# Performance work log

Measured on AMD Instinct MI355X. Metric: run time of the kernel, lower is better.

## Reference

```python
import jax, jax.numpy as jnp
import numpy as np

B = 131072
D_IN = 128
D_H = 128
DT = 1.0
LN_EPS = 1e-5


def setup_inputs() -> dict:
    key = jax.random.key(0)
    ks = jax.random.split(key, 12)
    s_in = 1.0 / np.sqrt(D_IN)
    s_h = 1.0 / np.sqrt(D_H)
    s_g = 1.0 / np.sqrt(D_IN + D_H)
    return {
        "x_t": jax.random.normal(ks[0], (B, D_IN), dtype=jnp.float32),
        "state": jax.random.normal(ks[1], (B, D_H), dtype=jnp.float32),
        "w_in": jax.random.uniform(ks[2], (D_H, D_IN), jnp.float32, -s_in, s_in),
        "b_in": jax.random.uniform(ks[3], (D_H,), jnp.float32, -s_in, s_in),
        "w_rec": jax.random.uniform(ks[4], (D_H, D_H), jnp.float32, -s_h, s_h),
        "w_gate": jax.random.uniform(ks[5], (D_H, D_IN + D_H), jnp.float32, -s_g, s_g),
        "b_gate": jax.random.uniform(ks[6], (D_H,), jnp.float32, -s_g, s_g),
        "bias": jnp.zeros((D_H,), jnp.float32),
        "log_step": jnp.zeros((D_H,), jnp.float32),
        "ln_gamma": jnp.ones((D_IN + D_H,), jnp.float32),
        "ln_beta": jnp.zeros((D_IN + D_H,), jnp.float32),
    }


def reference(x_t, state, w_in, b_in, w_rec, w_gate, b_gate, bias, log_step, ln_gamma, ln_beta):
    # per-unit learned time scale in (0, 1)
    step_size = jax.nn.sigmoid(log_step)  # [D_H]
    # drive = input_proj(x) + recurrent_proj(tanh(state)) + bias
    drive = (jnp.einsum("bi,hi->bh", x_t, w_in) + b_in
             + jnp.einsum("bj,hj->bh", jnp.tanh(state), w_rec)
             + bias)  # [B, D_H]
    # LayerNorm over concat([x, state])
    gi = jnp.concatenate([x_t, state], axis=-1)  # [B, D_IN+D_H]
    mu = jnp.mean(gi, axis=-1, keepdims=True)
    var = jnp.mean(jnp.square(gi - mu), axis=-1, keepdims=True)
    gi = (gi - mu) * jax.lax.rsqrt(var + LN_EPS) * ln_gamma + ln_beta
    gate = jax.nn.sigmoid(jnp.einsum("bk,hk->bh", gi, w_gate) + b_gate)  # [B, D_H]
    target = jnp.tanh(drive)
    blend = jnp.minimum(DT * step_size * gate, 1.0)
    new_state = state + blend * (target - state)
    return new_state
```

## Files before the change

### kernel.cpp

```cpp
#include <hip/hip_runtime.h>

#define D        128
#define M_TILE   32
#define THREADS  512
#define B_ROWS   131072
#define NTILES   (B_ROWS / M_TILE)
#define GRID     512

typedef __bf16  bf16x8  __attribute__((ext_vector_type(8)));
typedef float   f32x4   __attribute__((ext_vector_type(4)));

#define LOG2E 1.4426950408889634f
#define WS_FRAGS      4096
#define WS_PARAMS_OFF (2 * WS_FRAGS)
#define WS_NEEDED     (2 * WS_FRAGS * 16 + 128 * 16)

__device__ __forceinline__ float fexp2(float x) { return __builtin_amdgcn_exp2f(x); }
__device__ __forceinline__ float frcp(float x)  { return __builtin_amdgcn_rcpf(x); }

__device__ __forceinline__ float fast_tanh(float x) {
    float e = fexp2(x * (2.f * LOG2E));
    return 1.f - 2.f * frcp(e + 1.f);
}
__device__ __forceinline__ float fast_sigmoid(float x) {
    return frcp(1.f + fexp2(-LOG2E * x));
}

__global__ __launch_bounds__(THREADS)
void prep(const float* __restrict__ w_in,   const float* __restrict__ b_in,
          const float* __restrict__ w_rec,  const float* __restrict__ w_gate,
          const float* __restrict__ b_gate, const float* __restrict__ bias,
          const float* __restrict__ log_step,
          const float* __restrict__ gamma,  const float* __restrict__ beta,
          bf16x8* __restrict__ ws)
{
    const int bid = blockIdx.x, tid = threadIdx.x;
    if (bid < 8) {
        const int t    = bid * THREADS + tid;
        const int l    = t & 63;
        const int kb   = (t >> 6) & 7;
        const int w    = (t >> 9) & 7;
        const int hcol = w * 16 + (l & 15);
        const int k    = kb * 32 + ((l >> 4) & 3) * 8;
        bf16x8 fd, fg;
        const float* s1 = (k < 128) ? (w_in + hcol * 128 + k) : (w_rec + hcol * 128 + (k - 128));
        const float* s2 = w_gate + hcol * 256 + k;
        #pragma unroll
        for (int j = 0; j < 8; ++j) {
            fd[j] = (__bf16)s1[j];
            fg[j] = (__bf16)(s2[j] * gamma[k + j]);
        }
        ws[t]            = fd;
        ws[WS_FRAGS + t] = fg;
    } else {
        const int h   = tid >> 2;
        const int sub = tid & 3;
        float bacc = 0.f, csum = 0.f;
        const float* wp = w_gate + h * 256 + sub * 64;
        const float* gp = gamma + sub * 64;
        const float* bp = beta  + sub * 64;
        #pragma unroll
        for (int k = 0; k < 64; ++k) {
            const float wv = wp[k];
            bacc += wv * bp[k];
            csum += (float)(__bf16)(wv * gp[k]);
        }
        bacc += __shfl_xor(bacc, 1);
        bacc += __shfl_xor(bacc, 2);
        csum += __shfl_xor(csum, 1);
        csum += __shfl_xor(csum, 2);
        if (sub == 0) {
            f32x4 p;
            p[0] = fast_sigmoid(log_step[h]);
            p[1] = b_in[h] + bias[h];
            p[2] = b_gate[h] + bacc;
            p[3] = csum;
            *((f32x4*)(ws + WS_PARAMS_OFF) + h) = p;
        }
    }
}

__global__ __launch_bounds__(THREADS, 4)
void liquid_cell_ws(const float* __restrict__ x, const float* __restrict__ st,
                    const bf16x8* __restrict__ ws, float* __restrict__ out)
{
    __shared__ __align__(16) __bf16 XT[M_TILE * 128];
    __shared__ __align__(16) __bf16 TT[M_TILE * 128];
    __shared__ __align__(16) __bf16 SS[M_TILE * 128];
    __shared__ float2 MUB[M_TILE];

    const int tid  = threadIdx.x;
    const int lane = tid & 63;
    const int wave = tid >> 6;
    const int q    = lane >> 4;
    const int arow = lane & 15;
    const int hcol = wave * 16 + arow;
    const int koff = q * 8;
    const int fbase = wave * 512 + lane;

    const f32x4 pp = *((const f32x4*)(ws + WS_PARAMS_OFF) + hcol);
    const float stepv = pp[0], bd = pp[1], bg = pp[2], colsum = pp[3];

    const bf16x8* WD = ws;
    const bf16x8* WG = ws + WS_FRAGS;

    const int r    = tid >> 4;
    const int c0   = (tid & 15) * 8;
    const int sw   = (r & 7) << 3;
    const int rsw  = (arow & 7) << 3;

    for (int tile = blockIdx.x; tile < NTILES; tile += GRID) {
        const float* xp = x  + ((long)tile * M_TILE + r) * D + c0;
        const float* sp = st + ((long)tile * M_TILE + r) * D + c0;
        const f32x4 xa = *(const f32x4*)xp, xb = *(const f32x4*)(xp + 4);
        const f32x4 sa = *(const f32x4*)sp, sb = *(const f32x4*)(sp + 4);

        float sum = 0.f, sq = 0.f;
        #pragma unroll
        for (int j = 0; j < 4; ++j) {
            sum += xa[j] + xb[j] + sa[j] + sb[j];
            sq  += xa[j]*xa[j] + xb[j]*xb[j] + sa[j]*sa[j] + sb[j]*sb[j];
        }
        #pragma unroll
        for (int m = 1; m < 16; m <<= 1) {
            sum += __shfl_xor(sum, m);
            sq  += __shfl_xor(sq,  m);
        }
        const float mu   = sum * (1.f / 256.f);
        const float rstd = __builtin_amdgcn_rsqf(sq * (1.f / 256.f) - mu * mu + 1e-5f);

        bf16x8 fx, ft, fs;
        #pragma unroll
        for (int j = 0; j < 4; ++j) {
            fx[j]     = (__bf16)xa[j];
            fx[j + 4] = (__bf16)xb[j];
            ft[j]     = (__bf16)fast_tanh(sa[j]);
            ft[j + 4] = (__bf16)fast_tanh(sb[j]);
            fs[j]     = (__bf16)sa[j];
            fs[j + 4] = (__bf16)sb[j];
        }

        __syncthreads();
        *(bf16x8*)&XT[(r * 128 + c0) ^ sw] = fx;
        *(bf16x8*)&TT[(r * 128 + c0) ^ sw] = ft;
        *(bf16x8*)&SS[(r * 128 + c0) ^ sw] = fs;
        if ((tid & 15) == 0) MUB[r] = make_float2(mu * rstd, rstd);
        __syncthreads();

        bf16x8 fw[8], fv[8];
        #pragma unroll
        for (int kb = 0; kb < 8; ++kb) {
            fw[kb] = WG[fbase + kb * 64];
            fv[kb] = WD[fbase + kb * 64];
        }

        f32x4 acc2[2], acc1[2];
        acc2[0] = (f32x4)(0.f); acc2[1] = (f32x4)(0.f);
        acc1[0] = (f32x4)(0.f); acc1[1] = (f32x4)(0.f);
        #pragma unroll
        for (int ms = 0; ms < 2; ++ms) {
            const int base = (ms * 16 + arow) * 128;
            #pragma unroll
            for (int kb = 0; kb < 4; ++kb) {
                bf16x8 a = *(const bf16x8*)&XT[base + ((kb * 32 + koff) ^ rsw)];
                acc2[ms] = __builtin_amdgcn_mfma_f32_16x16x32_bf16(a, fw[kb], acc2[ms], 0, 0, 0);
                acc1[ms] = __builtin_amdgcn_mfma_f32_16x16x32_bf16(a, fv[kb], acc1[ms], 0, 0, 0);
            }
            #pragma unroll
            for (int kb = 0; kb < 4; ++kb) {
                bf16x8 s_ = *(const bf16x8*)&SS[base + ((kb * 32 + koff) ^ rsw)];
                acc2[ms] = __builtin_amdgcn_mfma_f32_16x16x32_bf16(s_, fw[kb + 4], acc2[ms], 0, 0, 0);
                bf16x8 t_ = *(const bf16x8*)&TT[base + ((kb * 32 + koff) ^ rsw)];
                acc1[ms] = __builtin_amdgcn_mfma_f32_16x16x32_bf16(t_, fv[kb + 4], acc1[ms], 0, 0, 0);
            }
        }

        const long obase = (long)tile * M_TILE;
        #pragma unroll
        for (int ms = 0; ms < 2; ++ms) {
            #pragma unroll
            for (int rg = 0; rg < 4; ++rg) {
                const int row = ms * 16 + q * 4 + rg;
                const float2 mr = MUB[row];
                const float gate   = fast_sigmoid(mr.y * acc2[ms][rg] - mr.x * colsum + bg);
                const float s      = (float)SS[(row * 128 + hcol) ^ ((row & 7) << 3)];
                const float target = fast_tanh(acc1[ms][rg] + bd);
                const float blend  = fminf(stepv * gate, 1.f);
                out[(obase + row) * D + hcol] = s + blend * (target - s);
            }
        }
    }
}

__global__ __launch_bounds__(THREADS, 4)
void liquid_cell_fb(const float* __restrict__ x,      const float* __restrict__ st,
                    const float* __restrict__ w_in,   const float* __restrict__ b_in,
                    const float* __restrict__ w_rec,  const float* __restrict__ w_gate,
                    const float* __restrict__ b_gate, const float* __restrict__ bias,
                    const float* __restrict__ log_step,
                    const float* __restrict__ gamma,  const float* __restrict__ beta,
                    float* __restrict__ out)
{
    __shared__ __align__(16) __bf16 A1[32 * 256];
    __shared__ __align__(16) __bf16 A2[32 * 256];
    __shared__ __align__(16) float  SBUF[32 * 128];

    const int tid  = threadIdx.x;
    const int lane = tid & 63;
    const int wave = tid >> 6;
    const int q    = lane >> 4;
    const int arow = lane & 15;
    const int hcol = wave * 16 + arow;
    const int koff = q * 8;

    const float stepv = fast_sigmoid(log_step[hcol]);
    const float bd    = b_in[hcol] + bias[hcol];
    float       bg    = b_gate[hcol];

    bf16x8 wd[8], wg[8];
    float betaAcc = 0.f;
    #pragma unroll
    for (int kb = 0; kb < 8; ++kb) {
        const int k = kb * 32 + koff;
        const float* s1 = (k < 128) ? (w_in  + hcol * 128 + k)
                                    : (w_rec + hcol * 128 + (k - 128));
        const float* s2 = w_gate + hcol * 256 + k;
        #pragma unroll
        for (int j = 0; j < 8; ++j) {
            wd[kb][j] = (__bf16)s1[j];
            const float wv = s2[j];
            wg[kb][j] = (__bf16)(wv * gamma[k + j]);
            betaAcc  += wv * beta[k + j];
        }
    }
    betaAcc += __shfl_xor(betaAcc, 16);
    betaAcc += __shfl_xor(betaAcc, 32);
    bg += betaAcc;

    const int r    = tid >> 4;
    const int c0   = (tid & 15) * 8;
    const int sw   = (r & 7) << 3;
    const int swf  = (r & 7) << 2;
    const int rsw  = (arow & 7) << 3;

    for (int tile = blockIdx.x; tile < (B_ROWS / 32); tile += GRID) {
        const float* xp = x  + ((long)tile * 32 + r) * D + c0;
        const float* sp = st + ((long)tile * 32 + r) * D + c0;
        const f32x4 xa = *(const f32x4*)xp, xb = *(const f32x4*)(xp + 4);
        const f32x4 sa = *(const f32x4*)sp, sb = *(const f32x4*)(sp + 4);

        float sum = 0.f, sq = 0.f;
        #pragma unroll
        for (int j = 0; j < 4; ++j) {
            sum += xa[j] + xb[j] + sa[j] + sb[j];
            sq  += xa[j]*xa[j] + xb[j]*xb[j] + sa[j]*sa[j] + sb[j]*sb[j];
        }
        #pragma unroll
        for (int m = 1; m < 16; m <<= 1) {
            sum += __shfl_xor(sum, m);
            sq  += __shfl_xor(sq,  m);
        }
        const float mu   = sum * (1.f / 256.f);
        const float rstd = __builtin_amdgcn_rsqf(sq * (1.f / 256.f) - mu * mu + 1e-5f);
        const float nmur = -mu * rstd;

        bf16x8 a1x, a1s, a2x, a2s;
        #pragma unroll
        for (int j = 0; j < 4; ++j) {
            a1x[j]     = (__bf16)xa[j];
            a1x[j + 4] = (__bf16)xb[j];
            a1s[j]     = (__bf16)fast_tanh(sa[j]);
            a1s[j + 4] = (__bf16)fast_tanh(sb[j]);
            a2x[j]     = (__bf16)(xa[j] * rstd + nmur);
            a2x[j + 4] = (__bf16)(xb[j] * rstd + nmur);
            a2s[j]     = (__bf16)(sa[j] * rstd + nmur);
            a2s[j + 4] = (__bf16)(sb[j] * rstd + nmur);
        }

        __syncthreads();
        *(bf16x8*)&A1[(r * 256 +       c0) ^ sw] = a1x;
        *(bf16x8*)&A1[(r * 256 + 128 + c0) ^ sw] = a1s;
        *(bf16x8*)&A2[(r * 256 +       c0) ^ sw] = a2x;
        *(bf16x8*)&A2[(r * 256 + 128 + c0) ^ sw] = a2s;
        *(f32x4*)&SBUF[(r * 128 + c0)     ^ swf] = sa;
        *(f32x4*)&SBUF[(r * 128 + c0 + 4) ^ swf] = sb;
        __syncthreads();

        f32x4 acc1[2], acc2[2];
        #pragma unroll
        for (int ms = 0; ms < 2; ++ms) { acc1[ms] = (f32x4)(0.f); acc2[ms] = (f32x4)(0.f); }

        #pragma unroll
        for (int ms = 0; ms < 2; ++ms) {
            const int base = (ms * 16 + arow) * 256;
            #pragma unroll
            for (int kb = 0; kb < 8; ++kb) {
                bf16x8 a = *(const bf16x8*)&A1[base + ((kb * 32 + koff) ^ rsw)];
                acc1[ms] = __builtin_amdgcn_mfma_f32_16x16x32_bf16(a, wd[kb], acc1[ms], 0, 0, 0);
            }
            #pragma unroll
            for (int kb = 0; kb < 8; ++kb) {
                bf16x8 a = *(const bf16x8*)&A2[base + ((kb * 32 + koff) ^ rsw)];
                acc2[ms] = __builtin_amdgcn_mfma_f32_16x16x32_bf16(a, wg[kb], acc2[ms], 0, 0, 0);
            }
        }

        const long obase = (long)tile * 32;
        #pragma unroll
        for (int ms = 0; ms < 2; ++ms) {
            #pragma unroll
            for (int rg = 0; rg < 4; ++rg) {
                const int row = ms * 16 + q * 4 + rg;
                const float s      = SBUF[(row * 128 + hcol) ^ ((row & 7) << 2)];
                const float target = fast_tanh(acc1[ms][rg] + bd);
                const float gate   = fast_sigmoid(acc2[ms][rg] + bg);
                const float blend  = fminf(stepv * gate, 1.f);
                out[(obase + row) * D + hcol] = s + blend * (target - s);
            }
        }
    }
}

extern "C" void kernel_launch(void* const* d_in, const int* in_sizes, int n_in,
                              void* d_out, int out_size, void* d_ws, size_t ws_size,
                              hipStream_t stream) {
    const float* x        = (const float*)d_in[0];
    const float* st       = (const float*)d_in[1];
    const float* w_in     = (const float*)d_in[2];
    const float* b_in     = (const float*)d_in[3];
    const float* w_rec    = (const float*)d_in[4];
    const float* w_gate   = (const float*)d_in[5];
    const float* b_gate   = (const float*)d_in[6];
    const float* bias     = (const float*)d_in[7];
    const float* log_step = (const float*)d_in[8];
    const float* gamma    = (const float*)d_in[9];
    const float* beta     = (const float*)d_in[10];
    float* out = (float*)d_out;

    if (ws_size >= (size_t)WS_NEEDED) {
        bf16x8* ws = (bf16x8*)d_ws;
        hipLaunchKernelGGL(prep, dim3(9), dim3(THREADS), 0, stream,
                           w_in, b_in, w_rec, w_gate, b_gate, bias,
                           log_step, gamma, beta, ws);
        hipLaunchKernelGGL(liquid_cell_ws, dim3(GRID), dim3(THREADS), 0, stream,
                           x, st, ws, out);
    } else {
        hipLaunchKernelGGL(liquid_cell_fb, dim3(GRID), dim3(THREADS), 0, stream,
                           x, st, w_in, b_in, w_rec, w_gate, b_gate, bias,
                           log_step, gamma, beta, out);
    }
}
```

Measured before the change: 57.25 us.

## Split waves into producer/consumer roles with double-buffered LDS tiles

Reworks the main kernel into a warp-specialized pipeline. Four producer waves load and normalize the next 32-row tile into one of two LDS buffers while four consumer waves run the MFMAs on the current buffer, each covering two column groups. The goal is to overlap global loads with matrix compute and cut one barrier per tile. The cost is half the waves issuing loads and half issuing MFMAs, more LDS per block, and weight fragments reloaded twice per tile by each consumer wave.

```diff
diff --git a/kernel.cpp b/kernel.cpp
--- a/kernel.cpp
+++ b/kernel.cpp
@@ -6,6 +6,7 @@
 #define B_ROWS   131072
 #define NTILES   (B_ROWS / M_TILE)
 #define GRID     512
+#define NT_PER   (NTILES / GRID)
 
 typedef __bf16  bf16x8  __attribute__((ext_vector_type(8)));
 typedef float   f32x4   __attribute__((ext_vector_type(4)));
@@ -25,6 +26,8 @@
 __device__ __forceinline__ float fast_sigmoid(float x) {
     return frcp(1.f + fexp2(-LOG2E * x));
 }
+
+#define MFMA(a, b, c) __builtin_amdgcn_mfma_f32_16x16x32_bf16((a), (b), (c), 0, 0, 0)
 
 __global__ __launch_bounds__(THREADS)
 void prep(const float* __restrict__ w_in,   const float* __restrict__ b_in,
@@ -81,79 +84,88 @@
 }
 
 __global__ __launch_bounds__(THREADS, 4)
-void liquid_cell_ws(const float* __restrict__ x, const float* __restrict__ st,
+void liquid_cell_pc(const float* __restrict__ x, const float* __restrict__ st,
                     const bf16x8* __restrict__ ws, float* __restrict__ out)
 {
-    __shared__ __align__(16) __bf16 XT[M_TILE * 128];
-    __shared__ __align__(16) __bf16 TT[M_TILE * 128];
-    __shared__ __align__(16) __bf16 SS[M_TILE * 128];
-    __shared__ float2 MUB[M_TILE];
+    __shared__ __align__(16) __bf16 XT[2][M_TILE * 128];
+    __shared__ __align__(16) __bf16 TT[2][M_TILE * 128];
+    __shared__ __align__(16) __bf16 SS[2][M_TILE * 128];
+    __shared__ float2 MUB[2][M_TILE];
 
     const int tid  = threadIdx.x;
     const int lane = tid & 63;
     const int wave = tid >> 6;
+    const bool producer = (wave < 4);
+
+    const int pr  = tid >> 3;
+    const int pc  = (tid & 7) * 16;
+    const int psw = (pr & 7) << 3;
+
     const int q    = lane >> 4;
     const int arow = lane & 15;
-    const int hcol = wave * 16 + arow;
     const int koff = q * 8;
-    const int fbase = wave * 512 + lane;
-
-    const f32x4 pp = *((const f32x4*)(ws + WS_PARAMS_OFF) + hcol);
-    const float stepv = pp[0], bd = pp[1], bg = pp[2], colsum = pp[3];
+    const int rsw  = (arow & 7) << 3;
+    const int cw   = wave - 4;
+    const int g0   = cw, g1 = cw + 4;
+    f32x4 pp0, pp1;
+    if (!producer) {
+        pp0 = *((const f32x4*)(ws + WS_PARAMS_OFF) + (g0 * 16 + arow));
+        pp1 = *((const f32x4*)(ws + WS_PARAMS_OFF) + (g1 * 16 + arow));
+    }
 
     const bf16x8* WD = ws;
     const bf16x8* WG = ws + WS_FRAGS;
 
-    const int r    = tid >> 4;
-    const int c0   = (tid & 15) * 8;
-    const int sw   = (r & 7) << 3;
-    const int rsw  = (arow & 7) << 3;
-
-    for (int tile = blockIdx.x; tile < NTILES; tile += GRID) {
-        const float* xp = x  + ((long)tile * M_TILE + r) * D + c0;
-        const float* sp = st + ((long)tile * M_TILE + r) * D + c0;
-        const f32x4 xa = *(const f32x4*)xp, xb = *(const f32x4*)(xp + 4);
-        const f32x4 sa = *(const f32x4*)sp, sb = *(const f32x4*)(sp + 4);
+    auto phaseA = [&](int b, long tile) {
+        const float* xr = x  + (tile * M_TILE + pr) * D + pc;
+        const float* sr = st + (tile * M_TILE + pr) * D + pc;
+        f32x4 xv0 = *(const f32x4*)xr,        xv1 = *(const f32x4*)(xr + 4);
+        f32x4 xv2 = *(const f32x4*)(xr + 8),  xv3 = *(const f32x4*)(xr + 12);
+        f32x4 sv0 = *(const f32x4*)sr,        sv1 = *(const f32x4*)(sr + 4);
+        f32x4 sv2 = *(const f32x4*)(sr + 8),  sv3 = *(const f32x4*)(sr + 12);
 
         float sum = 0.f, sq = 0.f;
         #pragma unroll
         for (int j = 0; j < 4; ++j) {
-            sum += xa[j] + xb[j] + sa[j] + sb[j];
-            sq  += xa[j]*xa[j] + xb[j]*xb[j] + sa[j]*sa[j] + sb[j]*sb[j];
-        }
-        #pragma unroll
-        for (int m = 1; m < 16; m <<= 1) {
+            sum += xv0[j] + xv1[j] + xv2[j] + xv3[j] + sv0[j] + sv1[j] + sv2[j] + sv3[j];
+            sq  += xv0[j]*xv0[j] + xv1[j]*xv1[j] + xv2[j]*xv2[j] + xv3[j]*xv3[j]
+                 + sv0[j]*sv0[j] + sv1[j]*sv1[j] + sv2[j]*sv2[j] + sv3[j]*sv3[j];
+        }
+        #pragma unroll
+        for (int m = 1; m < 8; m <<= 1) {
             sum += __shfl_xor(sum, m);
             sq  += __shfl_xor(sq,  m);
         }
         const float mu   = sum * (1.f / 256.f);
         const float rstd = __builtin_amdgcn_rsqf(sq * (1.f / 256.f) - mu * mu + 1e-5f);
 
-        bf16x8 fx, ft, fs;
+        bf16x8 fx0, fx1, ft0, ft1, fs0, fs1;
         #pragma unroll
         for (int j = 0; j < 4; ++j) {
-            fx[j]     = (__bf16)xa[j];
-            fx[j + 4] = (__bf16)xb[j];
-            ft[j]     = (__bf16)fast_tanh(sa[j]);
-            ft[j + 4] = (__bf16)fast_tanh(sb[j]);
-            fs[j]     = (__bf16)sa[j];
-            fs[j + 4] = (__bf16)sb[j];
-        }
-
-        __syncthreads();
-        *(bf16x8*)&XT[(r * 128 + c0) ^ sw] = fx;
-        *(bf16x8*)&TT[(r * 128 + c0) ^ sw] = ft;
-        *(bf16x8*)&SS[(r * 128 + c0) ^ sw] = fs;
-        if ((tid & 15) == 0) MUB[r] = make_float2(mu * rstd, rstd);
-        __syncthreads();
-
+            fx0[j] = (__bf16)xv0[j];  fx0[j + 4] = (__bf16)xv1[j];
+            fx1[j] = (__bf16)xv2[j];  fx1[j + 4] = (__bf16)xv3[j];
+            ft0[j] = (__bf16)fast_tanh(sv0[j]);  ft0[j + 4] = (__bf16)fast_tanh(sv1[j]);
+            ft1[j] = (__bf16)fast_tanh(sv2[j]);  ft1[j + 4] = (__bf16)fast_tanh(sv3[j]);
+            fs0[j] = (__bf16)sv0[j];  fs0[j + 4] = (__bf16)sv1[j];
+            fs1[j] = (__bf16)sv2[j];  fs1[j + 4] = (__bf16)sv3[j];
+        }
+        *(bf16x8*)&XT[b][(pr * 128 + pc)     ^ psw] = fx0;
+        *(bf16x8*)&XT[b][(pr * 128 + pc + 8) ^ psw] = fx1;
+        *(bf16x8*)&TT[b][(pr * 128 + pc)     ^ psw] = ft0;
+        *(bf16x8*)&TT[b][(pr * 128 + pc + 8) ^ psw] = ft1;
+        *(bf16x8*)&SS[b][(pr * 128 + pc)     ^ psw] = fs0;
+        *(bf16x8*)&SS[b][(pr * 128 + pc + 8) ^ psw] = fs1;
+        if ((tid & 7) == 0) MUB[b][pr] = make_float2(mu * rstd, rstd);
+    };
+
+    auto consume = [&](int b, long tile, int g, const f32x4& pp) {
+        const int fb = g * 512 + lane;
         bf16x8 fw[8], fv[8];
         #pragma unroll
         for (int kb = 0; kb < 8; ++kb) {
-            fw[kb] = WG[fbase + kb * 64];
-            fv[kb] = WD[fbase + kb * 64];
-        }
-
+            fw[kb] = WG[fb + kb * 64];
+            fv[kb] = WD[fb + kb * 64];
+        }
         f32x4 acc2[2], acc1[2];
         acc2[0] = (f32x4)(0.f); acc2[1] = (f32x4)(0.f);
         acc1[0] = (f32x4)(0.f); acc1[1] = (f32x4)(0.f);
@@ -162,33 +174,49 @@
             const int base = (ms * 16 + arow) * 128;
             #pragma unroll
             for (int kb = 0; kb < 4; ++kb) {
-                bf16x8 a = *(const bf16x8*)&XT[base + ((kb * 32 + koff) ^ rsw)];
-                acc2[ms] = __builtin_amdgcn_mfma_f32_16x16x32_bf16(a, fw[kb], acc2[ms], 0, 0, 0);
-                acc1[ms] = __builtin_amdgcn_mfma_f32_16x16x32_bf16(a, fv[kb], acc1[ms], 0, 0, 0);
+                bf16x8 a = *(const bf16x8*)&XT[b][base + ((kb * 32 + koff) ^ rsw)];
+                acc2[ms] = MFMA(a, fw[kb], acc2[ms]);
+                acc1[ms] = MFMA(a, fv[kb], acc1[ms]);
             }
             #pragma unroll
             for (int kb = 0; kb < 4; ++kb) {
-                bf16x8 s_ = *(const bf16x8*)&SS[base + ((kb * 32 + koff) ^ rsw)];
-                acc2[ms] = __builtin_amdgcn_mfma_f32_16x16x32_bf16(s_, fw[kb + 4], acc2[ms], 0, 0, 0);
-                bf16x8 t_ = *(const bf16x8*)&TT[base + ((kb * 32 + koff) ^ rsw)];
-                acc1[ms] = __builtin_amdgcn_mfma_f32_16x16x32_bf16(t_, fv[kb + 4], acc1[ms], 0, 0, 0);
-            }
-        }
-
-        const long obase = (long)tile * M_TILE;
+                bf16x8 s_ = *(const bf16x8*)&SS[b][base + ((kb * 32 + koff) ^ rsw)];
+                acc2[ms] = MFMA(s_, fw[kb + 4], acc2[ms]);
+                bf16x8 t_ = *(const bf16x8*)&TT[b][base + ((kb * 32 + koff) ^ rsw)];
+                acc1[ms] = MFMA(t_, fv[kb + 4], acc1[ms]);
+            }
+        }
+        const int  hcol  = g * 16 + arow;
+        const long obase = tile * M_TILE;
         #pragma unroll
         for (int ms = 0; ms < 2; ++ms) {
             #pragma unroll
             for (int rg = 0; rg < 4; ++rg) {
                 const int row = ms * 16 + q * 4 + rg;
-                const float2 mr = MUB[row];
-                const float gate   = fast_sigmoid(mr.y * acc2[ms][rg] - mr.x * colsum + bg);
-                const float s      = (float)SS[(row * 128 + hcol) ^ ((row & 7) << 3)];
-                const float target = fast_tanh(acc1[ms][rg] + bd);
-                const float blend  = fminf(stepv * gate, 1.f);
+                const float2 mr = MUB[b][row];
+                const float gate   = fast_sigmoid(mr.y * acc2[ms][rg] - mr.x * pp[3] + pp[2]);
+                const float s      = (float)SS[b][(row * 128 + hcol) ^ ((row & 7) << 3)];
+                const float target = fast_tanh(acc1[ms][rg] + pp[1]);
+                const float blend  = fminf(pp[0] * gate, 1.f);
                 out[(obase + row) * D + hcol] = s + blend * (target - s);
             }
         }
+    };
+
+    if (producer) phaseA(0, blockIdx.x);
+    __syncthreads();
+
+    #pragma unroll 1
+    for (int it = 0; it < NT_PER; ++it) {
+        const int  buf  = it & 1;
+        const long tile = (long)blockIdx.x + (long)it * GRID;
+        if (producer) {
+            if (it + 1 < NT_PER) phaseA(buf ^ 1, tile + GRID);
+        } else {
+            consume(buf, tile, g0, pp0);
+            consume(buf, tile, g1, pp1);
+        }
+        __syncthreads();
     }
 }
 
@@ -296,12 +324,12 @@
             #pragma unroll
             for (int kb = 0; kb < 8; ++kb) {
                 bf16x8 a = *(const bf16x8*)&A1[base + ((kb * 32 + koff) ^ rsw)];
-                acc1[ms] = __builtin_amdgcn_mfma_f32_16x16x32_bf16(a, wd[kb], acc1[ms], 0, 0, 0);
+                acc1[ms] = MFMA(a, wd[kb], acc1[ms]);
             }
             #pragma unroll
             for (int kb = 0; kb < 8; ++kb) {
                 bf16x8 a = *(const bf16x8*)&A2[base + ((kb * 32 + koff) ^ rsw)];
-                acc2[ms] = __builtin_amdgcn_mfma_f32_16x16x32_bf16(a, wg[kb], acc2[ms], 0, 0, 0);
+                acc2[ms] = MFMA(a, wg[kb], acc2[ms]);
             }
         }
 
@@ -342,7 +370,7 @@
         hipLaunchKernelGGL(prep, dim3(9), dim3(THREADS), 0, stream,
                            w_in, b_in, w_rec, w_gate, b_gate, bias,
                            log_step, gamma, beta, ws);
-        hipLaunchKernelGGL(liquid_cell_ws, dim3(GRID), dim3(THREADS), 0, stream,
+        hipLaunchKernelGGL(liquid_cell_pc, dim3(GRID), dim3(THREADS), 0, stream,
                            x, st, ws, out);
     } else {
         hipLaunchKernelGGL(liquid_cell_fb, dim3(GRID), dim3(THREADS), 0, stream,
```

New measurement: 132.6 us. 132% more time.
